# Kernel optimization log

Hardware: AMD Instinct MI355X
Metric: run time of the kernel (lower is better)

The kernel has to match this reference:

```python
import jax, jax.numpy as jnp
import numpy as np

B, T, E, NH = 2, 2048, 512, 8
HD = E // NH
SCALE = float(HD) ** -0.5


def setup_inputs() -> dict:
    key = jax.random.key(0)
    ks = jax.random.split(key, 7)
    s = 0.02
    return {
        "x": jax.random.normal(ks[0], (B, T, E), dtype=jnp.float32),
        "w_qkv": jax.random.normal(ks[1], (E, 3 * E), dtype=jnp.float32) * s,
        "b_qkv": jax.random.normal(ks[2], (3 * E,), dtype=jnp.float32) * s,
        "w_od": jax.random.normal(ks[3], (E, 2 * NH), dtype=jnp.float32) * s,
        "b_od": jax.random.normal(ks[4], (2 * NH,), dtype=jnp.float32) * s,
        "w_out": jax.random.normal(ks[5], (E, E), dtype=jnp.float32) * s,
        "b_out": jax.random.normal(ks[6], (E,), dtype=jnp.float32) * s,
    }


def _heads(t):  # (B,T,E) -> (B*NH, T, HD)
    return t.reshape(B, T, NH, HD).transpose(0, 2, 1, 3).reshape(B * NH, T, HD)


def _point_mask(idx, j):  # idx: (B*NH,T) float indices -> one-hot (B*NH,T,T)
    return (j[None, None, :] == idx[:, :, None]).astype(jnp.float32)


def reference(x, w_qkv, b_qkv, w_od, b_od, w_out, b_out):
    qkv = x @ w_qkv + b_qkv
    Q, K, V = jnp.split(qkv, 3, axis=-1)  # each (B,T,E)

    od = Q @ w_od + b_od  # (B,T,2*NH)
    offset, duration = jnp.split(od, 2, axis=-1)
    offset = jnp.tanh(offset) * T
    duration = jax.nn.sigmoid(duration) * T

    query_index = jnp.arange(T, dtype=x.dtype)[None, :, None]  # (1,T,1)
    anchor = query_index + offset  # (B,T,NH)
    # 'b t nh -> (b nh) t'
    anchor = anchor.transpose(0, 2, 1).reshape(B * NH, T)
    duration = duration.transpose(0, 2, 1).reshape(B * NH, T)

    start = anchor - duration
    end = anchor + duration
    bound_l = jnp.floor(start)
    bound_r = jnp.ceil(end)
    anchor_l = jnp.floor(anchor)
    anchor_r = anchor_l + 1.0

    j = jnp.arange(T, dtype=x.dtype)
    neg_bound_weight = (bound_l - start)[:, :, None] * _point_mask(bound_l, j) \
                     + (end - bound_r)[:, :, None] * _point_mask(bound_r, j)
    anchor_dist_l = anchor - anchor_l
    anchor_weight = anchor_dist_l[:, :, None] * _point_mask(anchor_r, j) \
                  + (1.0 - anchor_dist_l)[:, :, None] * _point_mask(anchor_l, j)
    point_weight = 1.0 + neg_bound_weight + anchor_weight  # (B*NH,T,T)

    # segment mask: True OUTSIDE [bound_l, bound_r]
    attn_mask = (j[None, None, :] < bound_l[:, :, None]) | (j[None, None, :] > bound_r[:, :, None])

    Qh, Kh, Vh = _heads(Q), _heads(K), _heads(V)  # (B*NH, T, HD)
    scores = jnp.einsum('bic,brc->bir', Qh, Kh) * SCALE * point_weight
    scores = jnp.where(attn_mask, jnp.asarray(-1e8, scores.dtype), scores)
    attn = jax.nn.softmax(scores, axis=-1)
    out = jnp.einsum('bir,brc->bic', attn, Vh)  # (B*NH,T,HD)
    out = out.reshape(B, NH, T, HD).transpose(0, 2, 1, 3).reshape(B, T, E)
    return out @ w_out + b_out
```

## Files before the change

kernel.cpp:

```cpp
#include <hip/hip_runtime.h>
#include <math.h>

typedef float vf4 __attribute__((ext_vector_type(4)));
typedef float f32x4 __attribute__((ext_vector_type(4)));
typedef short bf16x8 __attribute__((ext_vector_type(8)));
typedef short short4v __attribute__((ext_vector_type(4)));
typedef int int2v __attribute__((ext_vector_type(2)));
typedef int int4v __attribute__((ext_vector_type(4)));

constexpr int B = 2, T = 2048, E = 512, NH = 8, HD = 64;
constexpr int BH = B * NH;
constexpr int NT = BH * T;
constexpr int KSPLIT = 4;
constexpr float SCALE = 0.125f;
constexpr float LOG2E = 1.44269504088896f;
constexpr float QSC = SCALE * LOG2E;

static __device__ __forceinline__ short f2bf(float f) {
  unsigned u = __float_as_uint(f);
  unsigned r = (u + 0x7fffu + ((u >> 16) & 1u)) >> 16;
  return (short)r;
}
static __device__ __forceinline__ unsigned pk2bf(float a, float b) {
  unsigned lo = (unsigned)(unsigned short)f2bf(a);
  unsigned hi = (unsigned)(unsigned short)f2bf(b);
  return lo | (hi << 16);
}
static __device__ __forceinline__ unsigned pkhu(float a, float b) {
  unsigned ua = __float_as_uint(a) + 0x8000u;
  unsigned ub = __float_as_uint(b) + 0x8000u;
  return __builtin_amdgcn_perm(ub, ua, 0x07060302u);
}
#if __has_builtin(__builtin_amdgcn_exp2f)
#define EXP2F(x) __builtin_amdgcn_exp2f(x)
#else
#define EXP2F(x) exp2f(x)
#endif
static __device__ __forceinline__ float bf2f(short s) {
  return __uint_as_float(((unsigned)(unsigned short)s) << 16);
}

__global__ __launch_bounds__(256) void prep_all(
    const float* __restrict__ x, const float* __restrict__ w_qkv,
    const float* __restrict__ b_qkv, const float* __restrict__ w_od,
    const float* __restrict__ b_od,
    short* __restrict__ xb, short* __restrict__ wTq, short* __restrict__ wTo,
    const float* __restrict__ w_out, float* __restrict__ Wc,
    float* __restrict__ bc)
{
  __shared__ float sh[8464];
  const int bid = blockIdx.x;
  const int tid = threadIdx.x;

  if (bid < 2048) {
    int idx = (bid * 256 + tid) * 4;
    vf4 v = *(const vf4*)&x[idx];
    short4v o;
    o[0] = f2bf(v[0]); o[1] = f2bf(v[1]); o[2] = f2bf(v[2]); o[3] = f2bf(v[3]);
    *(short4v*)&xb[idx] = o;
  } else if (bid < 3072) {
    const float* w; short* wT; int N, t;
    if (bid < 2816) { t = bid - 2048; w = w_qkv; wT = wTq; N = 1536; }
    else            { t = bid - 2816; w = w_out; wT = wTo; N = 512; }
    float (*tt)[33] = (float(*)[33])sh;
    const int k0 = (t & 15) * 32;
    const int n0 = (t >> 4) * 32;
    const int c = tid & 31, r = tid >> 5;
#pragma unroll
    for (int p = 0; p < 4; ++p)
      tt[r + p * 8][c] = w[(size_t)(k0 + r + p * 8) * N + n0 + c];
    __syncthreads();
#pragma unroll
    for (int p = 0; p < 4; ++p)
      wT[(size_t)(n0 + r + p * 8) * 512 + k0 + c] = f2bf(tt[c][r + p * 8]);
  } else {
    float* Lod = sh;
    float (*pb)[17] = (float(*)[17])(sh + 8192);
    const int bx = bid - 3072;
#pragma unroll
    for (int p = 0; p < 8; ++p) {
      int idx = (p * 256 + tid) * 4;
      *(vf4*)&Lod[idx] = *(const vf4*)&w_od[idx];
    }
    __syncthreads();
    if (bx < 32) {
      const int k = bx * 16 + (tid >> 4);
      const int c = tid & 15;
      float s = 0.0f;
      for (int m = 0; m < E; m += 4) {
        vf4 wq = *(const vf4*)&w_qkv[(size_t)k * 1536 + m];
        s += wq[0] * Lod[(m + 0) * 16 + c] + wq[1] * Lod[(m + 1) * 16 + c]
           + wq[2] * Lod[(m + 2) * 16 + c] + wq[3] * Lod[(m + 3) * 16 + c];
      }
      Wc[k * 16 + c] = s;
    } else {
      const int c = tid & 15, seg = tid >> 4;
      float s = 0.0f;
      for (int m = seg * 32; m < seg * 32 + 32; ++m)
        s += b_qkv[m] * Lod[m * 16 + c];
      pb[seg][c] = s;
      __syncthreads();
      if (tid < 16) {
        float acc = b_od[tid];
#pragma unroll
        for (int g = 0; g < 16; ++g) acc += pb[g][tid];
        bc[tid] = acc;
      }
    }
  }
}

__global__ __launch_bounds__(256) void qkv_od(
    const short* __restrict__ xb, const short* __restrict__ wT,
    const float* __restrict__ bias, short* __restrict__ qkvb,
    short* __restrict__ Vtg,
    const float* __restrict__ x, const float* __restrict__ Wc,
    const float* __restrict__ bc, float* __restrict__ prm)
{
  __shared__ __align__(16) short smem_s[16896];
  const int bid = blockIdx.x;
  const int tid = threadIdx.x;

  if (bid < 768) {
    const int wave = tid >> 6, lane = tid & 63;
    const int quad = lane >> 4, l15 = lane & 15;
    const int wm = wave >> 1, wn = wave & 1;
    const int bx = bid % 24, by = bid / 24;
    const int m0 = by * 128, n0 = bx * 64;

    f32x4 acc[4][2];
#pragma unroll
    for (int mi = 0; mi < 4; ++mi)
#pragma unroll
      for (int ni = 0; ni < 2; ++ni) acc[mi][ni] = (f32x4){0, 0, 0, 0};

    const int sr = tid >> 1, sc = (tid & 1) * 16;
    const int br2 = tid >> 2, bk2 = (tid & 3) * 8;

#define QLD(R, K0) do {                                                   \
      R[0] = *(const bf16x8*)&xb[(size_t)(m0 + sr) * 512 + (K0) + sc];    \
      R[1] = *(const bf16x8*)&xb[(size_t)(m0 + sr) * 512 + (K0) + sc + 8];\
      R[2] = *(const bf16x8*)&wT[(size_t)(n0 + br2) * 512 + (K0) + bk2];  \
    } while (0)
#define QST(BUF, R) do {                                                  \
      short* As_ = smem_s + (BUF) * 7680;                                 \
      short* Bt_ = As_ + 5120;                                            \
      *(bf16x8*)&As_[sr * 40 + sc] = R[0];                                \
      *(bf16x8*)&As_[sr * 40 + sc + 8] = R[1];                            \
      *(bf16x8*)&Bt_[br2 * 40 + bk2] = R[2];                              \
    } while (0)
#define QMM(BUF) do {                                                     \
      const short* As_ = smem_s + (BUF) * 7680;                           \
      const short* Bt_ = As_ + 5120;                                      \
      bf16x8 aA[4], bB[2];                                                \
      for (int mi = 0; mi < 4; ++mi)                                      \
        aA[mi] = *(const bf16x8*)&As_[(wm * 64 + mi * 16 + l15) * 40 + quad * 8]; \
      for (int ni = 0; ni < 2; ++ni)                                      \
        bB[ni] = *(const bf16x8*)&Bt_[(wn * 32 + ni * 16 + l15) * 40 + quad * 8]; \
      for (int mi = 0; mi < 4; ++mi)                                      \
        for (int ni = 0; ni < 2; ++ni)                                    \
          acc[mi][ni] = __builtin_amdgcn_mfma_f32_16x16x32_bf16(          \
              aA[mi], bB[ni], acc[mi][ni], 0, 0, 0);                      \
    } while (0)

    bf16x8 rA[3], rB[3];
    QLD(rA, 0); QST(0, rA);
    QLD(rA, 32);
    __syncthreads();
#pragma unroll 1
    for (int k0 = 0; k0 < 512; k0 += 64) {
      if (k0 + 64 < 512) QLD(rB, k0 + 64);
      QMM(0);
      QST(1, rA);
      __syncthreads();
      if (k0 + 96 < 512) QLD(rA, k0 + 96);
      QMM(1);
      if (k0 + 64 < 512) { QST(0, rB); __syncthreads(); }
    }
#undef QLD
#undef QST
#undef QMM

#pragma unroll
    for (int mi = 0; mi < 4; ++mi)
#pragma unroll
      for (int ni = 0; ni < 2; ++ni) {
        const int col = n0 + wn * 32 + ni * 16 + l15;
        const int rowb = m0 + wm * 64 + mi * 16 + quad * 4;
        const float bs = bias[col];
        if (col < 1024) {
          const float qs = (col < 512) ? QSC : 1.0f;
#pragma unroll
          for (int r = 0; r < 4; ++r)
            qkvb[(size_t)(rowb + r) * 1536 + col] =
                f2bf((acc[mi][ni][r] + bs) * qs);
        } else {
          const int h = (col - 1024) >> 6, hd = col & 63;
          const int b = rowb >> 11, tt = rowb & 2047;
          int2v pk;
          pk[0] = (int)pk2bf(acc[mi][ni][0] + bs, acc[mi][ni][1] + bs);
          pk[1] = (int)pk2bf(acc[mi][ni][2] + bs, acc[mi][ni][3] + bs);
          *(int2v*)&Vtg[(size_t)(((b << 3) + h) * 64 + hd) * T + tt] = pk;
        }
      }
  } else {
    float* Lod = (float*)smem_s;
    float* ods = ((float*)smem_s) + 8192;
    const int obx = bid - 768;
#pragma unroll
    for (int p = 0; p < 8; ++p) {
      int idx = (p * 256 + tid) * 4;
      *(vf4*)&Lod[idx] = *(const vf4*)&Wc[idx];
    }
    __syncthreads();

    const int r = tid >> 4, c = tid & 15;
    const int row = obx * 16 + r;
    float sum = bc[c];
    const float* qr = x + (size_t)row * E;
    for (int k = 0; k < E; k += 4) {
      vf4 q = *(const vf4*)&qr[k];
      sum += q[0] * Lod[(k + 0) * 16 + c]
           + q[1] * Lod[(k + 1) * 16 + c]
           + q[2] * Lod[(k + 2) * 16 + c]
           + q[3] * Lod[(k + 3) * 16 + c];
    }
    ods[r * 16 + c] = sum;
    __syncthreads();

    if (tid < 128) {
      const int rr = tid >> 3, h = tid & 7;
      const int grow = obx * 16 + rr;
      const int b = grow / T, i = grow % T;
      float o = ods[rr * 16 + h];
      float d = ods[rr * 16 + h + 8];
      float offset   = tanhf(o) * (float)T;
      float duration = (float)T / (1.0f + expf(-d));
      float anchor = (float)i + offset;
      float start = anchor - duration;
      float end   = anchor + duration;
      float bl = floorf(start);
      float br = ceilf(end);
      float al = floorf(anchor);
      float wbl = bl - start;
      float wbr = end - br;
      float af  = anchor - al;
      float rsc = 1.0f;
      if (br < 0.0f || bl > (float)(T - 1)) {
        bl = 0.0f; br = (float)(T - 1);
        wbl = 0.0f; wbr = 0.0f; al = -5.0f; af = 0.0f;
        rsc = 0.0f;
      }
      int idx = (b * NH + h) * T + i;
      prm[0 * NT + idx] = bl;
      prm[1 * NT + idx] = br;
      prm[2 * NT + idx] = wbl;
      prm[3 * NT + idx] = wbr;
      prm[4 * NT + idx] = al;
      prm[5 * NT + idx] = af;
      prm[6 * NT + idx] = rsc;
    }
  }
}

__global__ __launch_bounds__(256, 4) void flash_attn_mfma7(
    const short* __restrict__ qkvb, const short* __restrict__ Vtg,
    const float* __restrict__ prm,
    short* __restrict__ Opart, float* __restrict__ lpart)
{
  __shared__ __align__(16) short Ks[2][64 * 72];
  __shared__ __align__(16) short Vt[2][64 * 72];
  __shared__ __align__(16) short Ps[4][16 * 72];
  __shared__ float u_s[8];

  const int tid = threadIdx.x;
  const int wave = tid >> 6, lane = tid & 63;
  const int quad = lane >> 4, l15 = lane & 15;
  const int qt = blockIdx.x, bh = blockIdx.y, ks = blockIdx.z;
  const int b = bh >> 3, h = bh & 7;
  const int i0 = qt * 64;
  const int i = i0 + wave * 16 + l15;

  const int pidx = bh * T + i;
  float blf = prm[0 * NT + pidx];
  float brf = prm[1 * NT + pidx];
  float wbl = prm[2 * NT + pidx];
  float wbr = prm[3 * NT + pidx];
  float alf = prm[4 * NT + pidx];
  float afr = prm[5 * NT + pidx];
  float rsc = prm[6 * NT + pidx];
  const int bli = (int)blf, widi = (int)brf - bli, ali = (int)alf;
  const unsigned widu = (unsigned)widi;
  const float a1 = 1.0f - afr;

  bf16x8 aQ0, aQ1;
  {
    size_t bq = (size_t)(b * T + i) * 1536 + h * 64;
    aQ0 = *(const bf16x8*)&qkvb[bq + quad * 8];
    aQ1 = *(const bf16x8*)&qkvb[bq + 32 + quad * 8];
    if (rsc == 0.0f) {
      bf16x8 z = {0, 0, 0, 0, 0, 0, 0, 0};
      aQ0 = z; aQ1 = z;
    }
  }

  float bmn = blf, bmx = brf;
#pragma unroll
  for (int d = 1; d < 64; d <<= 1) {
    bmn = fminf(bmn, __shfl_xor(bmn, d));
    bmx = fmaxf(bmx, __shfl_xor(bmx, d));
  }
  if (lane == 0) { u_s[wave * 2] = bmn; u_s[wave * 2 + 1] = bmx; }
  __syncthreads();
  bmn = fminf(fminf(u_s[0], u_s[2]), fminf(u_s[4], u_s[6]));
  bmx = fmaxf(fmaxf(u_s[1], u_s[3]), fmaxf(u_s[5], u_s[7]));
  const int ktlo = max(ks * 8, max(((int)bmn) >> 6, 0));
  const int kthi = min(ks * 8 + 7, min(((int)bmx) >> 6, T / 64 - 1));

  f32x4 o[4];
#pragma unroll
  for (int c = 0; c < 4; ++c) o[c] = (f32x4){0, 0, 0, 0};
  f32x4 lq = (f32x4){0, 0, 0, 0};
  const short BF1 = (short)0x3F80;
  const bf16x8 vone = {BF1, BF1, BF1, BF1, BF1, BF1, BF1, BF1};

  const int rq = tid >> 3, cb = (tid & 7) * 8;
  const short* kbase = qkvb + (size_t)b * T * 1536 + 512 + h * 64 + cb;
  const short* vbase = Vtg + (size_t)bh * 64 * T + cb;

  bf16x8 kr0, kr1, vr0, vr1;
  if (ktlo <= kthi) {
    const int j0 = ktlo * 64;
    kr0 = *(const bf16x8*)&kbase[(size_t)(j0 + rq) * 1536];
    kr1 = *(const bf16x8*)&kbase[(size_t)(j0 + 32 + rq) * 1536];
    vr0 = *(const bf16x8*)&vbase[(size_t)rq * T + j0];
    vr1 = *(const bf16x8*)&vbase[(size_t)(32 + rq) * T + j0];
    *(bf16x8*)&Ks[0][rq * 72 + cb] = kr0;
    *(bf16x8*)&Ks[0][(32 + rq) * 72 + cb] = kr1;
    *(bf16x8*)&Vt[0][rq * 72 + cb] = vr0;
    *(bf16x8*)&Vt[0][(32 + rq) * 72 + cb] = vr1;
  }
  __syncthreads();

  int buf = 0;
#pragma unroll 1
  for (int kt = ktlo; kt <= kthi; ++kt) {
    const int j0 = kt * 64;
    if (kt < kthi) {
      const int j1 = j0 + 64;
      kr0 = *(const bf16x8*)&kbase[(size_t)(j1 + rq) * 1536];
      kr1 = *(const bf16x8*)&kbase[(size_t)(j1 + 32 + rq) * 1536];
      vr0 = *(const bf16x8*)&vbase[(size_t)rq * T + j1];
      vr1 = *(const bf16x8*)&vbase[(size_t)(32 + rq) * T + j1];
    }

    const short* KsB = Ks[buf];
    const short* VtB = Vt[buf];

    f32x4 s[4];
#pragma unroll
    for (int nc = 0; nc < 4; ++nc) {
      const short* kb = &KsB[(nc * 16 + l15) * 72 + quad * 8];
      f32x4 a = (f32x4){0, 0, 0, 0};
      a = __builtin_amdgcn_mfma_f32_16x16x32_bf16(*(const bf16x8*)&kb[0],  aQ0, a, 0, 0, 0);
      a = __builtin_amdgcn_mfma_f32_16x16x32_bf16(*(const bf16x8*)&kb[32], aQ1, a, 0, 0, 0);
      s[nc] = a;
    }

    const int clean = (bli < j0) & (bli + widi > j0 + 63) &
                      ((ali > j0 + 63) | (ali + 1 < j0));
    if (__all(clean)) {
#pragma unroll
      for (int nc = 0; nc < 4; ++nc) {
        float p0 = EXP2F(s[nc][0]);
        float p1 = EXP2F(s[nc][1]);
        float p2 = EXP2F(s[nc][2]);
        float p3 = EXP2F(s[nc][3]);
        int2v pk;
        pk[0] = (int)pkhu(p0, p1);
        pk[1] = (int)pkhu(p2, p3);
        *(int2v*)&Ps[wave][l15 * 72 + nc * 16 + quad * 4] = pk;
      }
    } else {
      const int dq  = j0 + quad * 4 - bli;
      const int dq2 = j0 + quad * 4 - ali;
#pragma unroll
      for (int nc = 0; nc < 4; ++nc) {
        const int dn = dq + nc * 16, d2n = dq2 + nc * 16;
        float pr[4];
#pragma unroll
        for (int r = 0; r < 4; ++r) {
          int d = dn + r, d2 = d2n + r;
          float e  = (d == 0) ? wbl : ((d == widi) ? wbr : 0.0f);
          float aw = (d2 == 0) ? a1 : ((d2 == 1) ? afr : 0.0f);
          float w = 1.0f + e + aw;
          float v = s[nc][r] * w;
          v = ((unsigned)d <= widu) ? v : -115.0f;
          pr[r] = EXP2F(v);
        }
        int2v pk;
        pk[0] = (int)pkhu(pr[0], pr[1]);
        pk[1] = (int)pkhu(pr[2], pr[3]);
        *(int2v*)&Ps[wave][l15 * 72 + nc * 16 + quad * 4] = pk;
      }
    }

    bf16x8 bP0 = *(const bf16x8*)&Ps[wave][l15 * 72 + quad * 8];
    bf16x8 bP1 = *(const bf16x8*)&Ps[wave][l15 * 72 + 32 + quad * 8];
    lq = __builtin_amdgcn_mfma_f32_16x16x32_bf16(vone, bP0, lq, 0, 0, 0);
    lq = __builtin_amdgcn_mfma_f32_16x16x32_bf16(vone, bP1, lq, 0, 0, 0);
#pragma unroll
    for (int nc2 = 0; nc2 < 4; ++nc2) {
      const short* vb = &VtB[(nc2 * 16 + l15) * 72 + quad * 8];
      o[nc2] = __builtin_amdgcn_mfma_f32_16x16x32_bf16(
          *(const bf16x8*)&vb[0],  bP0, o[nc2], 0, 0, 0);
      o[nc2] = __builtin_amdgcn_mfma_f32_16x16x32_bf16(
          *(const bf16x8*)&vb[32], bP1, o[nc2], 0, 0, 0);
    }

    if (kt < kthi) {
      short* Kn = Ks[buf ^ 1];
      short* Vn = Vt[buf ^ 1];
      *(bf16x8*)&Kn[rq * 72 + cb] = kr0;
      *(bf16x8*)&Kn[(32 + rq) * 72 + cb] = kr1;
      *(bf16x8*)&Vn[rq * 72 + cb] = vr0;
      *(bf16x8*)&Vn[(32 + rq) * 72 + cb] = vr1;
      __syncthreads();
      buf ^= 1;
    }
  }

  if (lane < 16)
    lpart[ks * NT + bh * T + i] = lq[0];

  size_t ob = (size_t)ks * (B * T * E) + (size_t)(b * T + i) * E + h * 64;
#pragma unroll
  for (int nc2 = 0; nc2 < 4; ++nc2) {
    int2v pk;
    pk[0] = (int)pk2bf(o[nc2][0], o[nc2][1]);
    pk[1] = (int)pk2bf(o[nc2][2], o[nc2][3]);
    *(int2v*)&Opart[ob + nc2 * 16 + quad * 4] = pk;
  }
}

__global__ __launch_bounds__(256) void out_gemm_fused(
    const short* __restrict__ Opart, const float* __restrict__ lpart,
    const short* __restrict__ wT, const float* __restrict__ bias,
    float* __restrict__ Co)
{
  __shared__ __align__(16) short smem_o[10240];
  __shared__ float inv_s[64 * 8];

  const int tid = threadIdx.x;
  const int wave = tid >> 6, lane = tid & 63;
  const int quad = lane >> 4, l15 = lane & 15;
  const int wm = wave >> 1, wn = wave & 1;
  const int m0 = blockIdx.y * 64, n0 = blockIdx.x * 64;

#pragma unroll
  for (int p = 0; p < 2; ++p) {
    int e = p * 256 + tid;
    int row = e >> 3, hh = e & 7;
    int grow = m0 + row;
    int bb = grow >> 11, ii = grow & (T - 1);
    int lidx = ((bb << 3) + hh) * T + ii;
    float l = (lpart[lidx] + lpart[NT + lidx]) +
              (lpart[2 * NT + lidx] + lpart[3 * NT + lidx]);
    inv_s[e] = 1.0f / l;
  }
  __syncthreads();

  f32x4 acc[2][2];
#pragma unroll
  for (int mi = 0; mi < 2; ++mi)
#pragma unroll
    for (int ni = 0; ni < 2; ++ni) acc[mi][ni] = (f32x4){0, 0, 0, 0};

  const int ar = tid >> 2, akc = (tid & 3) * 8;
  constexpr size_t SLAB = (size_t)B * T * E;

#define OLD(R, K0) do {                                                  \
    size_t abase = (size_t)(m0 + ar) * 512 + (K0) + akc;                 \
    bf16x8 q0 = *(const bf16x8*)&Opart[abase];                           \
    bf16x8 q1 = *(const bf16x8*)&Opart[SLAB + abase];                    \
    bf16x8 q2 = *(const bf16x8*)&Opart[2 * SLAB + abase];                \
    bf16x8 q3 = *(const bf16x8*)&Opart[3 * SLAB + abase];                \
    float iv = inv_s[ar * 8 + (((K0) + akc) >> 6)];                      \
    float fa[8];                                                         \
    for (int j = 0; j < 8; ++j)                                          \
      fa[j] = ((bf2f(q0[j]) + bf2f(q1[j])) +                             \
               (bf2f(q2[j]) + bf2f(q3[j]))) * iv;                        \
    int4v pk_;                                                           \
    pk_[0] = (int)pk2bf(fa[0], fa[1]);                                   \
    pk_[1] = (int)pk2bf(fa[2], fa[3]);                                   \
    pk_[2] = (int)pk2bf(fa[4], fa[5]);                                   \
    pk_[3] = (int)pk2bf(fa[6], fa[7]);                                   \
    R0 = pk_;                                                            \
    R1 = *(const bf16x8*)&wT[(size_t)(n0 + ar) * 512 + (K0) + akc];      \
  } while (0)
#define OST(BUF) do {                                                    \
    short* As_ = smem_o + (BUF) * 5120;                                  \
    short* Bt_ = As_ + 2560;                                             \
    *(int4v*)&As_[ar * 40 + akc] = R0;                                   \
    *(bf16x8*)&Bt_[ar * 40 + akc] = R1;                                  \
  } while (0)
#define OMM(BUF) do {                                                    \
    const short* As_ = smem_o + (BUF) * 5120;                            \
    const short* Bt_ = As_ + 2560;                                       \
    bf16x8 aA[2], bB[2];                                                 \
    for (int mi = 0; mi < 2; ++mi)                                       \
      aA[mi] = *(const bf16x8*)&As_[(wm * 32 + mi * 16 + l15) * 40 + quad * 8]; \
    for (int ni = 0; ni < 2; ++ni)                                       \
      bB[ni] = *(const bf16x8*)&Bt_[(wn * 32 + ni * 16 + l15) * 40 + quad * 8]; \
    for (int mi = 0; mi < 2; ++mi)                                       \
      for (int ni = 0; ni < 2; ++ni)                                     \
        acc[mi][ni] = __builtin_amdgcn_mfma_f32_16x16x32_bf16(           \
            aA[mi], bB[ni], acc[mi][ni], 0, 0, 0);                       \
  } while (0)

  int4v R0; bf16x8 R1;
  OLD(, 0); OST(0);
  OLD(, 32);
  __syncthreads();
#pragma unroll 1
  for (int k0 = 0; k0 < 512; k0 += 64) {
    OMM(0);
    OST(1);
    __syncthreads();
    if (k0 + 64 < 512) OLD(, k0 + 64);
    OMM(1);
    if (k0 + 64 < 512) {
      OST(0);
      __syncthreads();
      if (k0 + 96 < 512) OLD(, k0 + 96);
    }
  }
#undef OLD
#undef OST
#undef OMM

#pragma unroll
  for (int mi = 0; mi < 2; ++mi)
#pragma unroll
    for (int ni = 0; ni < 2; ++ni)
#pragma unroll
      for (int r = 0; r < 4; ++r) {
        int row = m0 + wm * 32 + mi * 16 + quad * 4 + r;
        int col = n0 + wn * 32 + ni * 16 + l15;
        Co[(size_t)row * 512 + col] = acc[mi][ni][r] + bias[col];
      }
}

extern "C" void kernel_launch(void* const* d_in, const int* in_sizes, int n_in,
                              void* d_out, int out_size, void* d_ws, size_t ws_size,
                              hipStream_t stream)
{
  const float* x     = (const float*)d_in[0];
  const float* w_qkv = (const float*)d_in[1];
  const float* b_qkv = (const float*)d_in[2];
  const float* w_od  = (const float*)d_in[3];
  const float* b_od  = (const float*)d_in[4];
  const float* w_out = (const float*)d_in[5];
  const float* b_out = (const float*)d_in[6];
  float* out = (float*)d_out;

  char* w = (char*)d_ws;
  short* xb    = (short*)w;  w += (size_t)B * T * E * 2;
  short* wTq   = (short*)w;  w += (size_t)E * 3 * E * 2;
  short* wTo   = (short*)w;  w += (size_t)E * E * 2;
  short* qkvb  = (short*)w;  w += (size_t)B * T * 3 * E * 2;
  short* Vtg   = (short*)w;  w += (size_t)B * T * E * 2;
  float* Wc    = (float*)w;  w += (size_t)E * 16 * 4;
  float* bc    = (float*)w;  w += 256;
  float* prm   = (float*)w;  w += (size_t)7 * NT * 4;
  short* Opart = (short*)w;  w += (size_t)KSPLIT * B * T * E * 2;
  float* lpart = (float*)w;  w += (size_t)KSPLIT * NT * 4;

  prep_all<<<dim3(3105), 256, 0, stream>>>(
      x, w_qkv, b_qkv, w_od, b_od, xb, wTq, wTo, w_out, Wc, bc);

  qkv_od<<<dim3(1024), 256, 0, stream>>>(
      xb, wTq, b_qkv, qkvb, Vtg, x, Wc, bc, prm);

  flash_attn_mfma7<<<dim3(T / 64, BH, KSPLIT), 256, 0, stream>>>(
      qkvb, Vtg, prm, Opart, lpart);

  out_gemm_fused<<<dim3(E / 64, B * T / 64), 256, 0, stream>>>(
      Opart, lpart, wTo, b_out, out);
}
```

Measured before the change: 181.0 us.

## Fuse x bf16 conversion into QKV GEMM and compute softmax sums with scalar adds

Drops the separate x-to-bf16 pass from the prep kernel; the QKV GEMM now loads fp32 x directly and packs it to bf16 while writing to shared memory. This removes one global write and read of the activation tensor, at the cost of twice the global load bytes for x inside the GEMM and extra VALU packing work. The flash-attention kernel also replaces the ones-vector MFMA row-sum with per-lane scalar accumulation plus two cross-lane shuffles.

```diff
diff --git a/kernel.cpp b/kernel.cpp
--- a/kernel.cpp
+++ b/kernel.cpp
@@ -40,28 +40,21 @@
   return __uint_as_float(((unsigned)(unsigned short)s) << 16);
 }
 
-__global__ __launch_bounds__(256) void prep_all(
-    const float* __restrict__ x, const float* __restrict__ w_qkv,
-    const float* __restrict__ b_qkv, const float* __restrict__ w_od,
-    const float* __restrict__ b_od,
-    short* __restrict__ xb, short* __restrict__ wTq, short* __restrict__ wTo,
-    const float* __restrict__ w_out, float* __restrict__ Wc,
-    float* __restrict__ bc)
+__global__ __launch_bounds__(256) void prep_w(
+    const float* __restrict__ w_qkv, const float* __restrict__ b_qkv,
+    const float* __restrict__ w_od, const float* __restrict__ b_od,
+    const float* __restrict__ w_out,
+    short* __restrict__ wTq, short* __restrict__ wTo,
+    float* __restrict__ Wc, float* __restrict__ bc)
 {
   __shared__ float sh[8464];
   const int bid = blockIdx.x;
   const int tid = threadIdx.x;
 
-  if (bid < 2048) {
-    int idx = (bid * 256 + tid) * 4;
-    vf4 v = *(const vf4*)&x[idx];
-    short4v o;
-    o[0] = f2bf(v[0]); o[1] = f2bf(v[1]); o[2] = f2bf(v[2]); o[3] = f2bf(v[3]);
-    *(short4v*)&xb[idx] = o;
-  } else if (bid < 3072) {
+  if (bid < 1024) {
     const float* w; short* wT; int N, t;
-    if (bid < 2816) { t = bid - 2048; w = w_qkv; wT = wTq; N = 1536; }
-    else            { t = bid - 2816; w = w_out; wT = wTo; N = 512; }
+    if (bid < 768) { t = bid; w = w_qkv; wT = wTq; N = 1536; }
+    else           { t = bid - 768; w = w_out; wT = wTo; N = 512; }
     float (*tt)[33] = (float(*)[33])sh;
     const int k0 = (t & 15) * 32;
     const int n0 = (t >> 4) * 32;
@@ -76,7 +69,7 @@
   } else {
     float* Lod = sh;
     float (*pb)[17] = (float(*)[17])(sh + 8192);
-    const int bx = bid - 3072;
+    const int bx = bid - 1024;
 #pragma unroll
     for (int p = 0; p < 8; ++p) {
       int idx = (p * 256 + tid) * 4;
@@ -111,11 +104,11 @@
 }
 
 __global__ __launch_bounds__(256) void qkv_od(
-    const short* __restrict__ xb, const short* __restrict__ wT,
+    const float* __restrict__ x, const short* __restrict__ wT,
     const float* __restrict__ bias, short* __restrict__ qkvb,
     short* __restrict__ Vtg,
-    const float* __restrict__ x, const float* __restrict__ Wc,
-    const float* __restrict__ bc, float* __restrict__ prm)
+    const float* __restrict__ Wc, const float* __restrict__ bc,
+    float* __restrict__ prm)
 {
   __shared__ __align__(16) short smem_s[16896];
   const int bid = blockIdx.x;
@@ -134,20 +127,32 @@
 #pragma unroll
       for (int ni = 0; ni < 2; ++ni) acc[mi][ni] = (f32x4){0, 0, 0, 0};
 
-    const int sr = tid >> 1, sc = (tid & 1) * 16;
+    const int sr = tid >> 1, scf = (tid & 1) * 16;
     const int br2 = tid >> 2, bk2 = (tid & 3) * 8;
 
-#define QLD(R, K0) do {                                                   \
-      R[0] = *(const bf16x8*)&xb[(size_t)(m0 + sr) * 512 + (K0) + sc];    \
-      R[1] = *(const bf16x8*)&xb[(size_t)(m0 + sr) * 512 + (K0) + sc + 8];\
-      R[2] = *(const bf16x8*)&wT[(size_t)(n0 + br2) * 512 + (K0) + bk2];  \
+#define QLD(RF, RB, K0) do {                                              \
+      const float* xr_ = &x[(size_t)(m0 + sr) * 512 + (K0) + scf];        \
+      RF[0] = *(const vf4*)&xr_[0];                                       \
+      RF[1] = *(const vf4*)&xr_[4];                                       \
+      RF[2] = *(const vf4*)&xr_[8];                                       \
+      RF[3] = *(const vf4*)&xr_[12];                                      \
+      RB = *(const bf16x8*)&wT[(size_t)(n0 + br2) * 512 + (K0) + bk2];    \
     } while (0)
-#define QST(BUF, R) do {                                                  \
+#define QST(BUF, RF, RB) do {                                             \
       short* As_ = smem_s + (BUF) * 7680;                                 \
       short* Bt_ = As_ + 5120;                                            \
-      *(bf16x8*)&As_[sr * 40 + sc] = R[0];                                \
-      *(bf16x8*)&As_[sr * 40 + sc + 8] = R[1];                            \
-      *(bf16x8*)&Bt_[br2 * 40 + bk2] = R[2];                              \
+      int4v w0_, w1_;                                                     \
+      w0_[0] = (int)pk2bf(RF[0][0], RF[0][1]);                            \
+      w0_[1] = (int)pk2bf(RF[0][2], RF[0][3]);                            \
+      w0_[2] = (int)pk2bf(RF[1][0], RF[1][1]);                            \
+      w0_[3] = (int)pk2bf(RF[1][2], RF[1][3]);                            \
+      w1_[0] = (int)pk2bf(RF[2][0], RF[2][1]);                            \
+      w1_[1] = (int)pk2bf(RF[2][2], RF[2][3]);                            \
+      w1_[2] = (int)pk2bf(RF[3][0], RF[3][1]);                            \
+      w1_[3] = (int)pk2bf(RF[3][2], RF[3][3]);                            \
+      *(int4v*)&As_[sr * 40 + scf] = w0_;                                 \
+      *(int4v*)&As_[sr * 40 + scf + 8] = w1_;                             \
+      *(bf16x8*)&Bt_[br2 * 40 + bk2] = RB;                                \
     } while (0)
 #define QMM(BUF) do {                                                     \
       const short* As_ = smem_s + (BUF) * 7680;                           \
@@ -163,19 +168,20 @@
               aA[mi], bB[ni], acc[mi][ni], 0, 0, 0);                      \
     } while (0)
 
-    bf16x8 rA[3], rB[3];
-    QLD(rA, 0); QST(0, rA);
-    QLD(rA, 32);
+    vf4 fA[4], fB[4];
+    bf16x8 bA, bB2;
+    QLD(fA, bA, 0); QST(0, fA, bA);
+    QLD(fA, bA, 32);
     __syncthreads();
 #pragma unroll 1
     for (int k0 = 0; k0 < 512; k0 += 64) {
-      if (k0 + 64 < 512) QLD(rB, k0 + 64);
+      if (k0 + 64 < 512) QLD(fB, bB2, k0 + 64);
       QMM(0);
-      QST(1, rA);
+      QST(1, fA, bA);
       __syncthreads();
-      if (k0 + 96 < 512) QLD(rA, k0 + 96);
+      if (k0 + 96 < 512) QLD(fA, bA, k0 + 96);
       QMM(1);
-      if (k0 + 64 < 512) { QST(0, rB); __syncthreads(); }
+      if (k0 + 64 < 512) { QST(0, fB, bB2); __syncthreads(); }
     }
 #undef QLD
 #undef QST
@@ -263,7 +269,7 @@
   }
 }
 
-__global__ __launch_bounds__(256, 4) void flash_attn_mfma7(
+__global__ __launch_bounds__(256, 4) void flash_attn_mfma5(
     const short* __restrict__ qkvb, const short* __restrict__ Vtg,
     const float* __restrict__ prm,
     short* __restrict__ Opart, float* __restrict__ lpart)
@@ -320,9 +326,7 @@
   f32x4 o[4];
 #pragma unroll
   for (int c = 0; c < 4; ++c) o[c] = (f32x4){0, 0, 0, 0};
-  f32x4 lq = (f32x4){0, 0, 0, 0};
-  const short BF1 = (short)0x3F80;
-  const bf16x8 vone = {BF1, BF1, BF1, BF1, BF1, BF1, BF1, BF1};
+  float lacc = 0.0f;
 
   const int rq = tid >> 3, cb = (tid & 7) * 8;
   const short* kbase = qkvb + (size_t)b * T * 1536 + 512 + h * 64 + cb;
@@ -376,6 +380,7 @@
         float p1 = EXP2F(s[nc][1]);
         float p2 = EXP2F(s[nc][2]);
         float p3 = EXP2F(s[nc][3]);
+        lacc += (p0 + p1) + (p2 + p3);
         int2v pk;
         pk[0] = (int)pkhu(p0, p1);
         pk[1] = (int)pkhu(p2, p3);
@@ -396,7 +401,9 @@
           float w = 1.0f + e + aw;
           float v = s[nc][r] * w;
           v = ((unsigned)d <= widu) ? v : -115.0f;
-          pr[r] = EXP2F(v);
+          float p = EXP2F(v);
+          lacc += p;
+          pr[r] = p;
         }
         int2v pk;
         pk[0] = (int)pkhu(pr[0], pr[1]);
@@ -407,8 +414,6 @@
 
     bf16x8 bP0 = *(const bf16x8*)&Ps[wave][l15 * 72 + quad * 8];
     bf16x8 bP1 = *(const bf16x8*)&Ps[wave][l15 * 72 + 32 + quad * 8];
-    lq = __builtin_amdgcn_mfma_f32_16x16x32_bf16(vone, bP0, lq, 0, 0, 0);
-    lq = __builtin_amdgcn_mfma_f32_16x16x32_bf16(vone, bP1, lq, 0, 0, 0);
 #pragma unroll
     for (int nc2 = 0; nc2 < 4; ++nc2) {
       const short* vb = &VtB[(nc2 * 16 + l15) * 72 + quad * 8];
@@ -430,8 +435,10 @@
     }
   }
 
+  lacc += __shfl_xor(lacc, 16);
+  lacc += __shfl_xor(lacc, 32);
   if (lane < 16)
-    lpart[ks * NT + bh * T + i] = lq[0];
+    lpart[ks * NT + bh * T + i] = lacc;
 
   size_t ob = (size_t)ks * (B * T * E) + (size_t)(b * T + i) * E + h * 64;
 #pragma unroll
@@ -479,7 +486,7 @@
   const int ar = tid >> 2, akc = (tid & 3) * 8;
   constexpr size_t SLAB = (size_t)B * T * E;
 
-#define OLD(R, K0) do {                                                  \
+#define OLDF(K0) do {                                                    \
     size_t abase = (size_t)(m0 + ar) * 512 + (K0) + akc;                 \
     bf16x8 q0 = *(const bf16x8*)&Opart[abase];                           \
     bf16x8 q1 = *(const bf16x8*)&Opart[SLAB + abase];                    \
@@ -519,23 +526,23 @@
   } while (0)
 
   int4v R0; bf16x8 R1;
-  OLD(, 0); OST(0);
-  OLD(, 32);
+  OLDF(0); OST(0);
+  OLDF(32);
   __syncthreads();
 #pragma unroll 1
   for (int k0 = 0; k0 < 512; k0 += 64) {
     OMM(0);
     OST(1);
     __syncthreads();
-    if (k0 + 64 < 512) OLD(, k0 + 64);
+    if (k0 + 64 < 512) OLDF(k0 + 64);
     OMM(1);
     if (k0 + 64 < 512) {
       OST(0);
       __syncthreads();
-      if (k0 + 96 < 512) OLD(, k0 + 96);
-    }
-  }
-#undef OLD
+      if (k0 + 96 < 512) OLDF(k0 + 96);
+    }
+  }
+#undef OLDF
 #undef OST
 #undef OMM
 
@@ -565,7 +572,6 @@
   float* out = (float*)d_out;
 
   char* w = (char*)d_ws;
-  short* xb    = (short*)w;  w += (size_t)B * T * E * 2;
   short* wTq   = (short*)w;  w += (size_t)E * 3 * E * 2;
   short* wTo   = (short*)w;  w += (size_t)E * E * 2;
   short* qkvb  = (short*)w;  w += (size_t)B * T * 3 * E * 2;
@@ -576,13 +582,13 @@
   short* Opart = (short*)w;  w += (size_t)KSPLIT * B * T * E * 2;
   float* lpart = (float*)w;  w += (size_t)KSPLIT * NT * 4;
 
-  prep_all<<<dim3(3105), 256, 0, stream>>>(
-      x, w_qkv, b_qkv, w_od, b_od, xb, wTq, wTo, w_out, Wc, bc);
+  prep_w<<<dim3(1057), 256, 0, stream>>>(
+      w_qkv, b_qkv, w_od, b_od, w_out, wTq, wTo, Wc, bc);
 
   qkv_od<<<dim3(1024), 256, 0, stream>>>(
-      xb, wTq, b_qkv, qkvb, Vtg, x, Wc, bc, prm);
-
-  flash_attn_mfma7<<<dim3(T / 64, BH, KSPLIT), 256, 0, stream>>>(
+      x, wTq, b_qkv, qkvb, Vtg, Wc, bc, prm);
+
+  flash_attn_mfma5<<<dim3(T / 64, BH, KSPLIT), 256, 0, stream>>>(
       qkvb, Vtg, prm, Opart, lpart);
 
   out_gemm_fused<<<dim3(E / 64, B * T / 64), 256, 0, stream>>>(
```

After: 177.3 us. 2.0% less time.
